# Kernel tuning notes

Hardware: AMD Instinct MI355X
Metric: run time of the kernel (lower is better)

The kernel has to match this reference:

```python
import jax, jax.numpy as jnp
import numpy as np

B = 4
G = 1024                      # GridSize
H = 1.0 / (G - 1)             # h = (right-left)/(GridSize-1), area=[[0,0],[1,1]]
GD = 0.0                      # boundary value for hard_encode padding


def _cross(a):
    # sum of 4-neighborhood: matches conv2d with kernel [[0,.5,0],[.5,0,.5],[0,.5,0]] / 0.5
    return a[..., :-2, 1:-1] + a[..., 2:, 1:-1] + a[..., 1:-1, :-2] + a[..., 1:-1, 2:]


def _inner(a):
    return a[..., 1:-1, 1:-1]


def kappa(x, mu):
    # assumed parameterization (kappa undefined in source): exp(mu * x)
    return jnp.exp(mu * x)


def setup_inputs() -> dict:
    key = jax.random.key(0)
    k1, k2, k3, k4 = jax.random.split(key, 4)
    pre = jax.random.normal(k1, (B, 1, G - 2, G - 2), jnp.float32)
    f = jax.random.normal(k2, (B, 1, G, G), jnp.float32)
    mu = jax.random.uniform(k3, (1,), jnp.float32)
    prev_pre = jax.random.normal(k4, (B, 1, G, G), jnp.float32) * 0.1
    return {"pre": pre, "f": f, "mu": mu, "prev_pre": prev_pre, "maxiter": 20}


def reference(pre, f, mu, prev_pre, maxiter):
    # w = kappa(prev_pre, mu) is iteration-invariant -> hoist out of the loop
    w = kappa(prev_pre, mu)            # [B,1,G,G]
    w_in = _inner(w)                   # [B,1,G-2,G-2]
    force = _inner(f) * (H * H)
    # k3 conv: 0.5*cross + 2*center
    y3 = 0.5 * _cross(w) + 2.0 * w_in

    def step(y, _):
        u = jnp.pad(y, ((0, 0), (0, 0), (1, 1), (1, 1)), constant_values=GD)
        y1 = 0.5 * _cross(u) * w_in    # conv(u, k1) * w_inner
        y2 = 0.5 * _cross(w * u)       # conv(w*u, k2)
        return (force + y1 + y2) / y3, None

    # original: one jac_step, then `maxiter` more -> maxiter+1 total
    y, _ = jax.lax.scan(step, pre, None, length=maxiter + 1)
    return y
```

## Files before the change

### kernel.cpp

```cpp
#include <hip/hip_runtime.h>

#define BB 4
#define GG 1024
#define NI 1022
#define SROW 1024
#define HH2 (2.0f / (1023.0f * 1023.0f))
#define OFFC 12
#define TOUTC 104
#define NTC 10
#define HS 128

typedef float vf4 __attribute__((ext_vector_type(4)));
typedef float vf2 __attribute__((ext_vector_type(2)));

__device__ __forceinline__ float dpp_left(float x) {
    int i = __builtin_bit_cast(int, x);
    i = __builtin_amdgcn_update_dpp(i, i, 0x138, 0xf, 0xf, false);
    return __builtin_bit_cast(float, i);
}
__device__ __forceinline__ float dpp_right(float x) {
    int i = __builtin_bit_cast(int, x);
    i = __builtin_amdgcn_update_dpp(i, i, 0x130, 0xf, 0xf, false);
    return __builtin_bit_cast(float, i);
}

template<int TKP, int OFFR, int TOUTR, bool VIN4, bool VOUT4>
__global__ __launch_bounds__(1024, 8)
void pinn_slab(const float* __restrict__ ysrc,
               const float* __restrict__ fglob,
               const float* __restrict__ mu_p,
               const float* __restrict__ pp,
               float* __restrict__ yout)
{
    __shared__ float lds4[4][32 * HS];
    float* const wh0 = lds4[0];
    float* const wh1 = lds4[1];

    const int tid = threadIdx.x;
    const int tx = tid & 31, ty = tid >> 5;
    const int b  = blockIdx.z;
    const int AR = blockIdx.y * TOUTR - OFFR;
    const int A0 = blockIdx.x * TOUTC - OFFC;
    const int R  = 2 * ty;
    const int c0 = 4 * tx;
    const float mu = mu_p[0];

    const int cb = min(max(A0 + c0, 0), GG - 4);
    const size_t pb = (size_t)b * GG * GG;
    const int X  = AR + R;
    const int p1 = min(max(X + 1, 0), GG - 1);
    const int p2 = min(max(X + 2, 0), GG - 1);
    vf4 wc0 = *(const vf4*)&pp[pb + (size_t)p1 * GG + cb];
    vf4 wc1 = *(const vf4*)&pp[pb + (size_t)p2 * GG + cb];
    const vf4 fv0 = *(const vf4*)&fglob[pb + (size_t)p1 * GG + cb];
    const vf4 fv1 = *(const vf4*)&fglob[pb + (size_t)p2 * GG + cb];

    vf4 y0v, y1v;
    {
        const int i0 = min(max(X,     0), NI - 1);
        const int i1 = min(max(X + 1, 0), NI - 1);
        if (VIN4) {
            const int cy = min(max(A0 + c0, 0), SROW - 4);
            y0v = *(const vf4*)&ysrc[(size_t)(b * NI + i0) * SROW + cy];
            y1v = *(const vf4*)&ysrc[(size_t)(b * NI + i1) * SROW + cy];
        } else {
            const int cy  = min(max(A0 + c0, 0), NI - 2);
            const int cy2 = min(cy + 2, NI - 2);
            #define LDY(dst, ii) { \
                const size_t base_ = (size_t)(b * NI + (ii)) * NI; \
                const vf2 a_ = *(const vf2*)&ysrc[base_ + cy]; \
                const vf2 b_ = *(const vf2*)&ysrc[base_ + cy2]; \
                dst[0] = a_[0]; dst[1] = a_[1]; dst[2] = b_[0]; dst[3] = b_[1]; }
            LDY(y0v, i0) LDY(y1v, i1)
            #undef LDY
        }
    }

    #pragma unroll
    for (int m = 0; m < 4; ++m) {
        wc0[m] = __expf(mu * wc0[m]);
        wc1[m] = __expf(mu * wc1[m]);
    }
    *(vf4*)&wh0[ty * HS + c0] = wc0;
    *(vf4*)&wh1[ty * HS + c0] = wc1;
    __syncthreads();

    const int prv = max(ty - 1, 0)  * HS + c0;
    const int nxt = min(ty + 1, 31) * HS + c0;
    const vf4 wN = *(const vf4*)&wh1[prv];
    const vf4 wS = *(const vf4*)&wh0[nxt];

    const float s1N  = dpp_right(wN[0]);
    const float s1c0 = dpp_right(wc0[0]);
    const float s1c1 = dpp_right(wc1[0]);
    const float s1S  = dpp_right(wS[0]);
    const float s2c0 = dpp_right(wc0[1]);
    const float s2c1 = dpp_right(wc1[1]);
    const float sf0  = dpp_right(fv0[0]);
    const float sf1  = dpp_right(fv1[0]);

    vf4 bN0,bS0,bW0,bE0,bf0, bN1,bS1,bW1,bE1,bf1;

    #define COEFF(kk, N_, C_, S_, s1N_, s1C_, s1S_, s2C_, FV, SF, BN, BS, BW, BE, BF, YV) { \
        const vf4 wNl = {N_[1], N_[2], N_[3], s1N_}; \
        const vf4 wWl = C_; \
        const vf4 wCl = {C_[1], C_[2], C_[3], s1C_}; \
        const vf4 wEl = {C_[2], C_[3], s1C_, s2C_}; \
        const vf4 wSl = {S_[1], S_[2], S_[3], s1S_}; \
        const vf4 aN = wCl + wNl, aS = wCl + wSl, aW = wCl + wWl, aE = wCl + wEl; \
        const vf4 den = (aN + aS) + (aW + aE); \
        const int gi = X + (kk); \
        vf4 rd; \
        _Pragma("unroll") \
        for (int m = 0; m < 4; ++m) { \
            float x = __builtin_amdgcn_rcpf(den[m]); \
            x = x * (2.0f - den[m] * x); \
            const int gj = A0 + c0 + m; \
            const bool in = (gi >= 0) && (gi < NI) && (gj >= 0) && (gj < NI); \
            rd[m] = in ? x : 0.0f; \
            YV[m] = in ? YV[m] : 0.0f; \
        } \
        BN = aN * rd; BS = aS * rd; BW = aW * rd; BE = aE * rd; \
        const vf4 fC = {FV[1], FV[2], FV[3], SF}; \
        BF = (fC * rd) * HH2; }

    COEFF(0, wN,  wc0, wc1, s1N,  s1c0, s1c1, s2c0, fv0, sf0, bN0,bS0,bW0,bE0,bf0, y0v)
    COEFF(1, wc0, wc1, wS,  s1c0, s1c1, s1S,  s2c1, fv1, sf1, bN1,bS1,bW1,bE1,bf1, y1v)
    #undef COEFF

    const int tyo = ty * HS + c0;
    const int upo = max(ty - 1, 0)  * HS + c0;
    const int dno = min(ty + 1, 31) * HS + c0;

    for (int t = 1; t <= TKP; ++t) {
        float* tb = lds4[2 * (t & 1)];
        float* bb = lds4[2 * (t & 1) + 1];
        *(vf4*)&tb[tyo] = y0v;
        *(vf4*)&bb[tyo] = y1v;
        __syncthreads();
        const vf4 up = *(const vf4*)&bb[upo];
        const vf4 dn = *(const vf4*)&tb[dno];
        const vf4 yW0 = {dpp_left(y0v[3]), y0v[0], y0v[1], y0v[2]};
        const vf4 yW1 = {dpp_left(y1v[3]), y1v[0], y1v[1], y1v[2]};
        const vf4 yE0 = {y0v[1], y0v[2], y0v[3], dpp_right(y0v[0])};
        const vf4 yE1 = {y1v[1], y1v[2], y1v[3], dpp_right(y1v[0])};
        vf4 n0 = bf0; n0 += bN0 * up;  n0 += bS0 * y1v; n0 += bW0 * yW0; n0 += bE0 * yE0;
        vf4 n1 = bf1; n1 += bN1 * y0v; n1 += bS1 * dn;  n1 += bW1 * yW1; n1 += bE1 * yE1;
        y0v = n0; y1v = n1;
    }

    if (c0 >= OFFC && c0 < OFFC + TOUTC) {
        const int gj0 = A0 + c0;
        if (VOUT4) {
            #define STORE4(kk, YV) { \
                const int r = R + (kk); \
                if (r >= OFFR && r < OFFR + TOUTR) { \
                    const int gi = AR + r; \
                    if (gi < NI && gj0 <= SROW - 4) \
                        *(vf4*)&yout[(size_t)(b * NI + gi) * SROW + gj0] = YV; } }
            STORE4(0, y0v) STORE4(1, y1v)
            #undef STORE4
        } else {
            #define STORE(kk, YV) { \
                const int r = R + (kk); \
                if (r >= OFFR && r < OFFR + TOUTR) { \
                    const int gi = AR + r; \
                    if (gi < NI) { \
                        const size_t rb = (size_t)(b * NI + gi) * NI; \
                        if (gj0 + 3 < NI) { \
                            vf2 pa, pv; pa[0]=YV[0]; pa[1]=YV[1]; pv[0]=YV[2]; pv[1]=YV[3]; \
                            *(vf2*)&yout[rb + gj0] = pa; *(vf2*)&yout[rb + gj0 + 2] = pv; \
                        } else { \
                            _Pragma("unroll") \
                            for (int m = 0; m < 4; ++m) \
                                if (gj0 + m < NI) yout[rb + gj0 + m] = YV[m]; \
                        } \
                    } } }
            STORE(0, y0v) STORE(1, y1v)
            #undef STORE
        }
    }
}

extern "C" void kernel_launch(void* const* d_in, const int* in_sizes, int n_in,
                              void* d_out, int out_size, void* d_ws, size_t ws_size,
                              hipStream_t stream) {
    const float* pre = (const float*)d_in[0];
    const float* f   = (const float*)d_in[1];
    const float* mu  = (const float*)d_in[2];
    const float* pp  = (const float*)d_in[3];

    float* yA = (float*)d_ws;

    const dim3 bs(1024, 1, 1);
    pinn_slab<11, 11, 42, false, true ><<<dim3(NTC, 25, BB), bs, 0, stream>>>(pre, f, mu, pp, yA);
    pinn_slab<10, 10, 44, true,  false><<<dim3(NTC, 24, BB), bs, 0, stream>>>(yA,  f, mu, pp, (float*)d_out);
}
```

Baseline: 174.3 us.

## Pipeline w/f staging via async global-to-LDS loads across two column tiles

Blocks shrink to 512 threads, each holding four rows in registers, and every block now processes two column tiles in sequence. The w and f fields are staged into LDS with global_load_lds, and the loads for the second tile are issued while the first tile iterates. The aim is to hide global load latency behind the time-stepping loop and to cut LDS halo exchanges per row. In exchange each step now needs two barriers with explicit waitcnt, shared memory use is larger, and occupancy may drop.

```diff
diff --git a/kernel.cpp b/kernel.cpp
--- a/kernel.cpp
+++ b/kernel.cpp
@@ -8,10 +8,12 @@
 #define OFFC 12
 #define TOUTC 104
 #define NTC 10
-#define HS 128
 
 typedef float vf4 __attribute__((ext_vector_type(4)));
 typedef float vf2 __attribute__((ext_vector_type(2)));
+
+typedef __attribute__((address_space(3))) void lds_vt;
+typedef const __attribute__((address_space(1))) void gm_vt;
 
 __device__ __forceinline__ float dpp_left(float x) {
     int i = __builtin_bit_cast(int, x);
@@ -24,160 +26,195 @@
     return __builtin_bit_cast(float, i);
 }
 
+#define WG_BAR() do { \
+    asm volatile("s_waitcnt lgkmcnt(0)" ::: "memory"); \
+    __builtin_amdgcn_s_barrier(); \
+    asm volatile("" ::: "memory"); } while (0)
+
 template<int TKP, int OFFR, int TOUTR, bool VIN4, bool VOUT4>
-__global__ __launch_bounds__(1024, 8)
-void pinn_slab(const float* __restrict__ ysrc,
+__global__ __launch_bounds__(512, 4)
+void pinn_pipe(const float* __restrict__ ysrc,
                const float* __restrict__ fglob,
                const float* __restrict__ mu_p,
                const float* __restrict__ pp,
                float* __restrict__ yout)
 {
-    __shared__ float lds4[4][32 * HS];
-    float* const wh0 = lds4[0];
-    float* const wh1 = lds4[1];
-
-    const int tid = threadIdx.x;
-    const int tx = tid & 31, ty = tid >> 5;
-    const int b  = blockIdx.z;
-    const int AR = blockIdx.y * TOUTR - OFFR;
-    const int A0 = blockIdx.x * TOUTC - OFFC;
-    const int R  = 2 * ty;
-    const int c0 = 4 * tx;
+    __shared__ __align__(16) float smem[20480];
+    float* const wstg  = smem;
+    float* const fstg  = smem + 8192;
+    float* const ytopb = smem + 16384;
+    float* const ybotb = smem + 18432;
+
+    const int tid  = threadIdx.x;
+    const int tx   = tid & 31, ty = tid >> 5;
+    const int wvid = tid >> 6;
+    const int ln   = tid & 63;
+    const int b    = blockIdx.z;
+    const int AR   = blockIdx.y * TOUTR - OFFR;
+    const int R    = 4 * ty, c0 = 4 * tx;
     const float mu = mu_p[0];
-
-    const int cb = min(max(A0 + c0, 0), GG - 4);
     const size_t pb = (size_t)b * GG * GG;
-    const int X  = AR + R;
-    const int p1 = min(max(X + 1, 0), GG - 1);
-    const int p2 = min(max(X + 2, 0), GG - 1);
-    vf4 wc0 = *(const vf4*)&pp[pb + (size_t)p1 * GG + cb];
-    vf4 wc1 = *(const vf4*)&pp[pb + (size_t)p2 * GG + cb];
-    const vf4 fv0 = *(const vf4*)&fglob[pb + (size_t)p1 * GG + cb];
-    const vf4 fv1 = *(const vf4*)&fglob[pb + (size_t)p2 * GG + cb];
-
-    vf4 y0v, y1v;
-    {
-        const int i0 = min(max(X,     0), NI - 1);
-        const int i1 = min(max(X + 1, 0), NI - 1);
-        if (VIN4) {
-            const int cy = min(max(A0 + c0, 0), SROW - 4);
-            y0v = *(const vf4*)&ysrc[(size_t)(b * NI + i0) * SROW + cy];
-            y1v = *(const vf4*)&ysrc[(size_t)(b * NI + i1) * SROW + cy];
-        } else {
-            const int cy  = min(max(A0 + c0, 0), NI - 2);
-            const int cy2 = min(cy + 2, NI - 2);
-            #define LDY(dst, ii) { \
-                const size_t base_ = (size_t)(b * NI + (ii)) * NI; \
-                const vf2 a_ = *(const vf2*)&ysrc[base_ + cy]; \
-                const vf2 b_ = *(const vf2*)&ysrc[base_ + cy2]; \
-                dst[0] = a_[0]; dst[1] = a_[1]; dst[2] = b_[0]; dst[3] = b_[1]; }
-            LDY(y0v, i0) LDY(y1v, i1)
-            #undef LDY
-        }
-    }
-
-    #pragma unroll
-    for (int m = 0; m < 4; ++m) {
-        wc0[m] = __expf(mu * wc0[m]);
-        wc1[m] = __expf(mu * wc1[m]);
-    }
-    *(vf4*)&wh0[ty * HS + c0] = wc0;
-    *(vf4*)&wh1[ty * HS + c0] = wc1;
-    __syncthreads();
-
-    const int prv = max(ty - 1, 0)  * HS + c0;
-    const int nxt = min(ty + 1, 31) * HS + c0;
-    const vf4 wN = *(const vf4*)&wh1[prv];
-    const vf4 wS = *(const vf4*)&wh0[nxt];
-
-    const float s1N  = dpp_right(wN[0]);
-    const float s1c0 = dpp_right(wc0[0]);
-    const float s1c1 = dpp_right(wc1[0]);
-    const float s1S  = dpp_right(wS[0]);
-    const float s2c0 = dpp_right(wc0[1]);
-    const float s2c1 = dpp_right(wc1[1]);
-    const float sf0  = dpp_right(fv0[0]);
-    const float sf1  = dpp_right(fv1[0]);
-
-    vf4 bN0,bS0,bW0,bE0,bf0, bN1,bS1,bW1,bE1,bf1;
-
-    #define COEFF(kk, N_, C_, S_, s1N_, s1C_, s1S_, s2C_, FV, SF, BN, BS, BW, BE, BF, YV) { \
-        const vf4 wNl = {N_[1], N_[2], N_[3], s1N_}; \
-        const vf4 wWl = C_; \
-        const vf4 wCl = {C_[1], C_[2], C_[3], s1C_}; \
-        const vf4 wEl = {C_[2], C_[3], s1C_, s2C_}; \
-        const vf4 wSl = {S_[1], S_[2], S_[3], s1S_}; \
-        const vf4 aN = wCl + wNl, aS = wCl + wSl, aW = wCl + wWl, aE = wCl + wEl; \
-        const vf4 den = (aN + aS) + (aW + aE); \
-        const int gi = X + (kk); \
-        vf4 rd; \
-        _Pragma("unroll") \
-        for (int m = 0; m < 4; ++m) { \
-            float x = __builtin_amdgcn_rcpf(den[m]); \
-            x = x * (2.0f - den[m] * x); \
-            const int gj = A0 + c0 + m; \
-            const bool in = (gi >= 0) && (gi < NI) && (gj >= 0) && (gj < NI); \
-            rd[m] = in ? x : 0.0f; \
-            YV[m] = in ? YV[m] : 0.0f; \
-        } \
-        BN = aN * rd; BS = aS * rd; BW = aW * rd; BE = aE * rd; \
-        const vf4 fC = {FV[1], FV[2], FV[3], SF}; \
-        BF = (fC * rd) * HH2; }
-
-    COEFF(0, wN,  wc0, wc1, s1N,  s1c0, s1c1, s2c0, fv0, sf0, bN0,bS0,bW0,bE0,bf0, y0v)
-    COEFF(1, wc0, wc1, wS,  s1c0, s1c1, s1S,  s2c1, fv1, sf1, bN1,bS1,bW1,bE1,bf1, y1v)
-    #undef COEFF
-
-    const int tyo = ty * HS + c0;
-    const int upo = max(ty - 1, 0)  * HS + c0;
-    const int dno = min(ty + 1, 31) * HS + c0;
-
-    for (int t = 1; t <= TKP; ++t) {
-        float* tb = lds4[2 * (t & 1)];
-        float* bb = lds4[2 * (t & 1) + 1];
-        *(vf4*)&tb[tyo] = y0v;
-        *(vf4*)&bb[tyo] = y1v;
+    const int X    = AR + R;
+
+    auto stage = [&](int A0) {
+        const int scol = min(max(A0 + (ln & 31) * 4, 0), GG - 4);
+        #pragma unroll
+        for (int i = 0; i < 4; ++i) {
+            const int j = (i * 8 + wvid) * 2 + (ln >> 5);
+            const int g = min(max(AR + 1 + j, 0), GG - 1);
+            const size_t go = pb + (size_t)g * GG + scol;
+            __builtin_amdgcn_global_load_lds((gm_vt*)&pp[go],
+                (lds_vt*)(wstg + (i * 8 + wvid) * 256), 16, 0, 0);
+            __builtin_amdgcn_global_load_lds((gm_vt*)&fglob[go],
+                (lds_vt*)(fstg + (i * 8 + wvid) * 256), 16, 0, 0);
+        }
+    };
+
+    stage(2 * blockIdx.x * TOUTC - OFFC);
+
+    const int tyo = ty * 128 + c0;
+    const int upo = max(ty - 1, 0)  * 128 + c0;
+    const int dno = min(ty + 1, 15) * 128 + c0;
+
+    for (int tt = 0; tt < 2; ++tt) {
+        const int A0 = (2 * blockIdx.x + tt) * TOUTC - OFFC;
+
+        vf4 y0v, y1v, y2v, y3v;
+        {
+            const int i0 = min(max(X,     0), NI - 1);
+            const int i1 = min(max(X + 1, 0), NI - 1);
+            const int i2 = min(max(X + 2, 0), NI - 1);
+            const int i3 = min(max(X + 3, 0), NI - 1);
+            if (VIN4) {
+                const int cy = min(max(A0 + c0, 0), SROW - 4);
+                y0v = *(const vf4*)&ysrc[(size_t)(b * NI + i0) * SROW + cy];
+                y1v = *(const vf4*)&ysrc[(size_t)(b * NI + i1) * SROW + cy];
+                y2v = *(const vf4*)&ysrc[(size_t)(b * NI + i2) * SROW + cy];
+                y3v = *(const vf4*)&ysrc[(size_t)(b * NI + i3) * SROW + cy];
+            } else {
+                const int cy  = min(max(A0 + c0, 0), NI - 2);
+                const int cy2 = min(cy + 2, NI - 2);
+                #define LDY(dst, ii) { \
+                    const size_t base_ = (size_t)(b * NI + (ii)) * NI; \
+                    const vf2 a_ = *(const vf2*)&ysrc[base_ + cy]; \
+                    const vf2 b_ = *(const vf2*)&ysrc[base_ + cy2]; \
+                    dst[0] = a_[0]; dst[1] = a_[1]; dst[2] = b_[0]; dst[3] = b_[1]; }
+                LDY(y0v, i0) LDY(y1v, i1) LDY(y2v, i2) LDY(y3v, i3)
+                #undef LDY
+            }
+        }
+
         __syncthreads();
-        const vf4 up = *(const vf4*)&bb[upo];
-        const vf4 dn = *(const vf4*)&tb[dno];
-        const vf4 yW0 = {dpp_left(y0v[3]), y0v[0], y0v[1], y0v[2]};
-        const vf4 yW1 = {dpp_left(y1v[3]), y1v[0], y1v[1], y1v[2]};
-        const vf4 yE0 = {y0v[1], y0v[2], y0v[3], dpp_right(y0v[0])};
-        const vf4 yE1 = {y1v[1], y1v[2], y1v[3], dpp_right(y1v[0])};
-        vf4 n0 = bf0; n0 += bN0 * up;  n0 += bS0 * y1v; n0 += bW0 * yW0; n0 += bE0 * yE0;
-        vf4 n1 = bf1; n1 += bN1 * y0v; n1 += bS1 * dn;  n1 += bW1 * yW1; n1 += bE1 * yE1;
-        y0v = n0; y1v = n1;
-    }
-
-    if (c0 >= OFFC && c0 < OFFC + TOUTC) {
-        const int gj0 = A0 + c0;
-        if (VOUT4) {
-            #define STORE4(kk, YV) { \
-                const int r = R + (kk); \
-                if (r >= OFFR && r < OFFR + TOUTR) { \
-                    const int gi = AR + r; \
-                    if (gi < NI && gj0 <= SROW - 4) \
-                        *(vf4*)&yout[(size_t)(b * NI + gi) * SROW + gj0] = YV; } }
-            STORE4(0, y0v) STORE4(1, y1v)
-            #undef STORE4
-        } else {
-            #define STORE(kk, YV) { \
-                const int r = R + (kk); \
-                if (r >= OFFR && r < OFFR + TOUTR) { \
-                    const int gi = AR + r; \
-                    if (gi < NI) { \
-                        const size_t rb = (size_t)(b * NI + gi) * NI; \
-                        if (gj0 + 3 < NI) { \
-                            vf2 pa, pv; pa[0]=YV[0]; pa[1]=YV[1]; pv[0]=YV[2]; pv[1]=YV[3]; \
-                            *(vf2*)&yout[rb + gj0] = pa; *(vf2*)&yout[rb + gj0 + 2] = pv; \
-                        } else { \
-                            _Pragma("unroll") \
-                            for (int m = 0; m < 4; ++m) \
-                                if (gj0 + m < NI) yout[rb + gj0 + m] = YV[m]; \
-                        } \
-                    } } }
-            STORE(0, y0v) STORE(1, y1v)
-            #undef STORE
+
+        #pragma unroll
+        for (int u = 0; u < 4; ++u) {
+            vf4 w = *(const vf4*)&wstg[(R + u) * 128 + c0];
+            #pragma unroll
+            for (int m = 0; m < 4; ++m) w[m] = __expf(mu * w[m]);
+            *(vf4*)&wstg[(R + u) * 128 + c0] = w;
+        }
+        __syncthreads();
+
+        vf4 bN0,bS0,bW0,bE0,bf0, bN1,bS1,bW1,bE1,bf1,
+            bN2,bS2,bW2,bE2,bf2, bN3,bS3,bW3,bE3,bf3;
+
+        #define COEFF(kk, BN, BS, BW, BE, BF, YV) { \
+            const int jN = max(R + (kk) - 1, 0); \
+            const int jC = R + (kk); \
+            const int jS = min(R + (kk) + 1, 63); \
+            const int ce = min(c0 + 4, 124); \
+            const vf4 n4 = *(const vf4*)&wstg[jN * 128 + c0]; \
+            const vf2 n2 = *(const vf2*)&wstg[jN * 128 + ce]; \
+            const vf4 c4 = *(const vf4*)&wstg[jC * 128 + c0]; \
+            const vf2 c2 = *(const vf2*)&wstg[jC * 128 + ce]; \
+            const vf4 s4 = *(const vf4*)&wstg[jS * 128 + c0]; \
+            const vf2 s2 = *(const vf2*)&wstg[jS * 128 + ce]; \
+            const vf4 wN = {n4[1], n4[2], n4[3], n2[0]}; \
+            const vf4 wW = c4; \
+            const vf4 wC = {c4[1], c4[2], c4[3], c2[0]}; \
+            const vf4 wE = {c4[2], c4[3], c2[0], c2[1]}; \
+            const vf4 wS = {s4[1], s4[2], s4[3], s2[0]}; \
+            const vf4 aN = wC + wN, aS = wC + wS, aW = wC + wW, aE = wC + wE; \
+            const vf4 den = (aN + aS) + (aW + aE); \
+            const int gi = X + (kk); \
+            vf4 rd; \
+            _Pragma("unroll") \
+            for (int m = 0; m < 4; ++m) { \
+                float x = __builtin_amdgcn_rcpf(den[m]); \
+                x = x * (2.0f - den[m] * x); \
+                const int gj = A0 + c0 + m; \
+                const bool in = (gi >= 0) && (gi < NI) && (gj >= 0) && (gj < NI); \
+                rd[m] = in ? x : 0.0f; \
+                YV[m] = in ? YV[m] : 0.0f; \
+            } \
+            BN = aN * rd; BS = aS * rd; BW = aW * rd; BE = aE * rd; \
+            const vf4 f4 = *(const vf4*)&fstg[jC * 128 + c0]; \
+            const float f1 = fstg[jC * 128 + min(c0 + 4, 127)]; \
+            const vf4 fC = {f4[1], f4[2], f4[3], f1}; \
+            BF = (fC * rd) * HH2; }
+
+        COEFF(0, bN0,bS0,bW0,bE0,bf0, y0v)
+        COEFF(1, bN1,bS1,bW1,bE1,bf1, y1v)
+        COEFF(2, bN2,bS2,bW2,bE2,bf2, y2v)
+        COEFF(3, bN3,bS3,bW3,bE3,bf3, y3v)
+        #undef COEFF
+
+        __syncthreads();
+
+        if (tt == 0) stage((2 * blockIdx.x + 1) * TOUTC - OFFC);
+
+        for (int t = 1; t <= TKP; ++t) {
+            *(vf4*)&ytopb[tyo] = y0v;
+            *(vf4*)&ybotb[tyo] = y3v;
+            WG_BAR();
+            const vf4 up = *(const vf4*)&ybotb[upo];
+            const vf4 dn = *(const vf4*)&ytopb[dno];
+            WG_BAR();
+            const vf4 yW0 = {dpp_left(y0v[3]), y0v[0], y0v[1], y0v[2]};
+            const vf4 yW1 = {dpp_left(y1v[3]), y1v[0], y1v[1], y1v[2]};
+            const vf4 yW2 = {dpp_left(y2v[3]), y2v[0], y2v[1], y2v[2]};
+            const vf4 yW3 = {dpp_left(y3v[3]), y3v[0], y3v[1], y3v[2]};
+            const vf4 yE0 = {y0v[1], y0v[2], y0v[3], dpp_right(y0v[0])};
+            const vf4 yE1 = {y1v[1], y1v[2], y1v[3], dpp_right(y1v[0])};
+            const vf4 yE2 = {y2v[1], y2v[2], y2v[3], dpp_right(y2v[0])};
+            const vf4 yE3 = {y3v[1], y3v[2], y3v[3], dpp_right(y3v[0])};
+            vf4 n0 = bf0; n0 += bN0 * up;  n0 += bS0 * y1v; n0 += bW0 * yW0; n0 += bE0 * yE0;
+            vf4 n1 = bf1; n1 += bN1 * y0v; n1 += bS1 * y2v; n1 += bW1 * yW1; n1 += bE1 * yE1;
+            vf4 n2 = bf2; n2 += bN2 * y1v; n2 += bS2 * y3v; n2 += bW2 * yW2; n2 += bE2 * yE2;
+            vf4 n3 = bf3; n3 += bN3 * y2v; n3 += bS3 * dn;  n3 += bW3 * yW3; n3 += bE3 * yE3;
+            y0v = n0; y1v = n1; y2v = n2; y3v = n3;
+        }
+
+        if (c0 >= OFFC && c0 < OFFC + TOUTC) {
+            const int gj0 = A0 + c0;
+            if (VOUT4) {
+                #define STORE4(kk, YV) { \
+                    const int r = R + (kk); \
+                    if (r >= OFFR && r < OFFR + TOUTR) { \
+                        const int gi = AR + r; \
+                        if (gi < NI && gj0 <= SROW - 4) \
+                            *(vf4*)&yout[(size_t)(b * NI + gi) * SROW + gj0] = YV; } }
+                STORE4(0, y0v) STORE4(1, y1v) STORE4(2, y2v) STORE4(3, y3v)
+                #undef STORE4
+            } else {
+                #define STORE(kk, YV) { \
+                    const int r = R + (kk); \
+                    if (r >= OFFR && r < OFFR + TOUTR) { \
+                        const int gi = AR + r; \
+                        if (gi < NI) { \
+                            const size_t rb = (size_t)(b * NI + gi) * NI; \
+                            if (gj0 + 3 < NI) { \
+                                vf2 pa, pv; pa[0]=YV[0]; pa[1]=YV[1]; pv[0]=YV[2]; pv[1]=YV[3]; \
+                                *(vf2*)&yout[rb + gj0] = pa; *(vf2*)&yout[rb + gj0 + 2] = pv; \
+                            } else { \
+                                _Pragma("unroll") \
+                                for (int m = 0; m < 4; ++m) \
+                                    if (gj0 + m < NI) yout[rb + gj0 + m] = YV[m]; \
+                            } \
+                        } } }
+                STORE(0, y0v) STORE(1, y1v) STORE(2, y2v) STORE(3, y3v)
+                #undef STORE
+            }
         }
     }
 }
@@ -192,7 +229,7 @@
 
     float* yA = (float*)d_ws;
 
-    const dim3 bs(1024, 1, 1);
-    pinn_slab<11, 11, 42, false, true ><<<dim3(NTC, 25, BB), bs, 0, stream>>>(pre, f, mu, pp, yA);
-    pinn_slab<10, 10, 44, true,  false><<<dim3(NTC, 24, BB), bs, 0, stream>>>(yA,  f, mu, pp, (float*)d_out);
-}
+    const dim3 bs(512, 1, 1);
+    pinn_pipe<11, 11, 42, false, true ><<<dim3(NTC/2, 25, BB), bs, 0, stream>>>(pre, f, mu, pp, yA);
+    pinn_pipe<10, 10, 44, true,  false><<<dim3(NTC/2, 24, BB), bs, 0, stream>>>(yA,  f, mu, pp, (float*)d_out);
+}
```

New measurement: 172.9 us. Within noise of the previous version (-0.8%).
